# Optimization experiments

Hardware: AMD Instinct MI355X
Metric: run time of the kernel (lower is better)

Reference implementation:

```python
import jax, jax.numpy as jnp
import numpy as np

C = 256; GC = 32; G = C // GC; K = 3; S = 1; NEW = 2; PAD = (K - 1) // 2
IN1 = C * K * 2 + C * K * K // 32          # 1608
OUT1 = G * NEW * NEW * K * K // 4          # 72
OUT2 = G * NEW * NEW * K * K               # 288
B = 8; H = 56; W = 56


def setup_inputs():
    key = jax.random.key(0)
    k0, k1, k2 = jax.random.split(key, 3)
    inputs = jax.random.normal(k0, (B, C, H, W), jnp.float32)
    W1 = jax.random.normal(k1, (OUT1, IN1), jnp.float32) * np.float32(1.0 / np.sqrt(IN1))
    b1 = jnp.zeros((OUT1,), jnp.float32)
    W2 = jax.random.normal(k2, (OUT2, OUT1), jnp.float32) * np.float32(1.0 / np.sqrt(OUT1))
    b2 = jnp.zeros((OUT2,), jnp.float32)
    return {"inputs": inputs, "W1": W1, "b1": b1, "W2": W2, "b2": b2}


def _unfold(x, h, w):
    # torch.nn.Unfold(K, 1, PAD, S): patches of shape (B, C, K, K, h, w)
    xp = jnp.pad(x, ((0, 0), (0, 0), (PAD, PAD), (PAD, PAD)))
    cols = [xp[:, :, di:di + (h - 1) * S + 1:S, dj:dj + (w - 1) * S + 1:S]
            for di in range(K) for dj in range(K)]  # fixed K*K=9 slices
    return jnp.stack(cols, axis=2).reshape(x.shape[0], x.shape[1], K, K, h, w)


def reference(inputs, W1, b1, W2, b2):
    b, c, Hh, Ww = inputs.shape
    h = (Hh + 2 * PAD - K) // S + 1
    w = (Ww + 2 * PAD - K) // S + 1
    # (B, G, GC, K, K, h, w)
    x = _unfold(inputs, h, w).reshape(b, G, GC, K, K, h, w)
    # three max-pooled descriptors over different axes
    x1 = x.reshape(b, G, -1, GC // 32, K, K, h, w).max(axis=2).reshape(b, -1, h, w)  # (B, C*K*K//32, h, w)
    x2 = x.max(axis=3).reshape(b, -1, h, w)  # (B, C*K, h, w)
    x3 = x.max(axis=4).reshape(b, -1, h, w)  # (B, C*K, h, w)
    feat = jnp.concatenate([x1, x2, x3], axis=1)  # (B, IN1, h, w)
    # two biased 1x1 convs (ConvModule with no norm/act)
    y = jnp.einsum('bchw,oc->bohw', feat, W1) + b1[None, :, None, None]
    y = jnp.einsum('bchw,oc->bohw', y, W2) + b2[None, :, None, None]
    # softmax over the K*K kernel-window dim
    wgt = jax.nn.softmax(y.reshape(b, G, K * K, NEW * NEW, h, w), axis=2)
    # softmax-weighted local aggregation: sum over kernel window
    agg = jnp.einsum('bgckhw,bgknhw->bgcnhw', x.reshape(b, G, GC, K * K, h, w), wgt)
    # fold with non-overlapping (NEW, NEW) blocks == block upsampling reshape
    return agg.reshape(b, C, NEW, NEW, h, w).transpose(0, 1, 4, 2, 5, 3).reshape(b, C, h * NEW, w * NEW)
```

## Files before the change

### kernel.cpp

```cpp
#include <hip/hip_runtime.h>

#define CC   256
#define HH   56
#define WWID 56
#define KIN1 1608
#define KP1  1632
#define NO1  72
#define NO2  288
#define PPB  14
#define H2   112
#define W2D  112

typedef unsigned short u16;
typedef unsigned int   u32;
typedef __attribute__((ext_vector_type(8))) short v8s;
typedef __attribute__((ext_vector_type(4))) float v4f;

#define W1BF_ELEMS (80 * KP1)
#define W2BF_OFF_B 262144

#define LDS_TOTAL 40192
#define OFF_A 0
#define OFF_B 24832
#define OFF_C 33280
#define OFF_D 36608

__device__ __forceinline__ u16 f2b(float x) {
  u32 u = __float_as_uint(x);
  u = (u + 0x7FFFu + ((u >> 16) & 1u)) >> 16;
  return (u16)u;
}

__global__ void kConvW(const float* __restrict__ W1, const float* __restrict__ W2,
                       u16* __restrict__ w1bf, u16* __restrict__ w2bf) {
  int idx = blockIdx.x * 256 + threadIdx.x;
  if (idx < W1BF_ELEMS) {
    int m = idx / KP1, k = idx - m * KP1;
    float v = 0.f;
    if (m < NO1) {
      int orig = -1;
      if (k < 768)                 orig = 72 + (k & 255) * 3 + (k >> 8);
      else if (k < 1536)           orig = 840 + (k & 255) * 3 + ((k - 768) >> 8);
      else if ((k - 1536) < NO1)   orig = k - 1536;
      if (orig >= 0) v = W1[m * KIN1 + orig];
    }
    w1bf[idx] = f2b(v);
  } else {
    int i2 = idx - W1BF_ELEMS;
    if (i2 < NO2 * 96) {
      int m = i2 / 96, k = i2 - m * 96;
      w2bf[i2] = (k < NO1) ? f2b(W2[m * NO1 + k]) : (u16)0;
    }
  }
}

__global__ __launch_bounds__(256, 4)
void kFused(const float* __restrict__ in, const u16* __restrict__ w1bf,
            const float* __restrict__ b1, const u16* __restrict__ w2bf,
            const float* __restrict__ b2, float* __restrict__ out) {
  __shared__ __align__(16) char lds[LDS_TOTAL];
  u16*   rowmaxT = (u16*)(lds + OFF_A);
  u16*   colmaxT = (u16*)(lds + OFF_B);
  u16*   x1T     = (u16*)(lds + OFF_C);
  float* gmax_s  = (float*)(lds + OFF_D);
  float* partA   = (float*)(lds + OFF_A);
  float* y2L     = (float*)(lds + OFF_A);
  float* tile    = (float*)(lds + OFF_B);

  const int t  = threadIdx.x;
  const int jt = blockIdx.x, i = blockIdx.y, b = blockIdx.z;
  const int j0 = jt * PPB;
  const int c  = t;
  const int g  = c >> 5;
  const int gc = c & 31;
  const int w  = t >> 6, lane = t & 63;
  const int ml = lane & 15, quad = lane >> 4;

  {
    u32* xu = (u32*)x1T;
    if (t < 132) {
#pragma unroll
      for (int rp2 = 0; rp2 < 2; ++rp2) {
        int idx = 2 * t + rp2;
        if (idx < 192) { int row = idx / 12; xu[row * 52 + 36 + (idx - row * 12)] = 0u; }
        else { int e = idx - 192; xu[(14 + e / 36) * 52 + (e % 36)] = 0u; }
      }
    }
  }

  const float* rowbase0 = in + ((size_t)b * CC + c) * (HH * WWID);
  u32 win_p[3][8];
  float colmax[16];
#pragma unroll
  for (int k = 0; k < 16; ++k) colmax[k] = -3.0e38f;

#pragma unroll
  for (int r = 0; r < 3; ++r) {
    const int row = i - 1 + r;
    float sc[16];
    if (row < 0 || row >= HH) {
#pragma unroll
      for (int k = 0; k < 16; ++k) sc[k] = 0.f;
    } else {
      const float* rp = rowbase0 + row * WWID;
      float l[20];
      if (jt == 0) {
        const float4 a0 = *(const float4*)(rp), a1 = *(const float4*)(rp + 4),
                     a2 = *(const float4*)(rp + 8), a3 = *(const float4*)(rp + 12);
        l[0]=a0.x;l[1]=a0.y;l[2]=a0.z;l[3]=a0.w; l[4]=a1.x;l[5]=a1.y;l[6]=a1.z;l[7]=a1.w;
        l[8]=a2.x;l[9]=a2.y;l[10]=a2.z;l[11]=a2.w; l[12]=a3.x;l[13]=a3.y;l[14]=a3.z;l[15]=a3.w;
        sc[0] = 0.f;
#pragma unroll
        for (int k = 1; k < 16; ++k) sc[k] = l[k - 1];
      } else if (jt == 3) {
        const float* q = rp + 40;
        const float4 a0 = *(const float4*)(q), a1 = *(const float4*)(q + 4),
                     a2 = *(const float4*)(q + 8), a3 = *(const float4*)(q + 12);
        l[0]=a0.x;l[1]=a0.y;l[2]=a0.z;l[3]=a0.w; l[4]=a1.x;l[5]=a1.y;l[6]=a1.z;l[7]=a1.w;
        l[8]=a2.x;l[9]=a2.y;l[10]=a2.z;l[11]=a2.w; l[12]=a3.x;l[13]=a3.y;l[14]=a3.z;l[15]=a3.w;
#pragma unroll
        for (int k = 0; k < 15; ++k) sc[k] = l[k + 1];
        sc[15] = 0.f;
      } else {
        const float* q = rp + ((jt == 1) ? 12 : 24);
        const float4 a0 = *(const float4*)(q), a1 = *(const float4*)(q + 4),
                     a2 = *(const float4*)(q + 8), a3 = *(const float4*)(q + 12),
                     a4 = *(const float4*)(q + 16);
        l[0]=a0.x;l[1]=a0.y;l[2]=a0.z;l[3]=a0.w; l[4]=a1.x;l[5]=a1.y;l[6]=a1.z;l[7]=a1.w;
        l[8]=a2.x;l[9]=a2.y;l[10]=a2.z;l[11]=a2.w; l[12]=a3.x;l[13]=a3.y;l[14]=a3.z;l[15]=a3.w;
        l[16]=a4.x;l[17]=a4.y;l[18]=a4.z;l[19]=a4.w;
        if (jt == 1) {
#pragma unroll
          for (int k = 0; k < 16; ++k) sc[k] = l[k + 1];
        } else {
#pragma unroll
          for (int k = 0; k < 16; ++k) sc[k] = l[k + 3];
        }
      }
    }
#pragma unroll
    for (int k = 0; k < 16; ++k) colmax[k] = fmaxf(colmax[k], sc[k]);
#pragma unroll
    for (int n = 0; n < 14; ++n)
      rowmaxT[n * 776 + r * 256 + c] = f2b(fmaxf(fmaxf(sc[n], sc[n + 1]), sc[n + 2]));
#pragma unroll
    for (int col = 0; col < 16; ++col) {
      float m = sc[col];
      m = fmaxf(m, __shfl_xor(m, 1));
      m = fmaxf(m, __shfl_xor(m, 2));
      m = fmaxf(m, __shfl_xor(m, 4));
      m = fmaxf(m, __shfl_xor(m, 8));
      m = fmaxf(m, __shfl_xor(m, 16));
      if (gc == col) gmax_s[g * 48 + r * 16 + col] = m;
    }
#pragma unroll
    for (int k = 0; k < 8; ++k)
      win_p[r][k] = (u32)f2b(sc[2 * k]) | ((u32)f2b(sc[2 * k + 1]) << 16);
  }
#pragma unroll
  for (int col = 0; col < 16; ++col)
    colmaxT[col * 264 + c] = f2b(colmax[col]);
  asm volatile("s_waitcnt lgkmcnt(0)" ::: "memory");
#pragma unroll
  for (int rep = 0; rep < 4; ++rep) {
    int idx = gc + 32 * rep;
    if (idx < 126) {
      int n = idx / 9, r9 = idx - n * 9, ki = r9 / 3, kj = r9 - ki * 3;
      x1T[n * 104 + g * 9 + r9] = f2b(gmax_s[g * 48 + ki * 16 + n + kj]);
    }
  }
  __syncthreads();

  v4f acc[5];
#pragma unroll
  for (int mt = 0; mt < 5; ++mt) acc[mt] = (v4f){0.f, 0.f, 0.f, 0.f};
  const int ks0 = w * 13, ks1 = (w == 3) ? 51 : ks0 + 13;

  auto loadB = [&](int ks) -> v8s {
    if (ks < 24) {
      int kj = ks >> 3, c0 = (ks & 7) * 32;
      return *(v8s*)&colmaxT[(ml + kj) * 264 + c0 + quad * 8];
    } else if (ks < 48) {
      return *(v8s*)&rowmaxT[ml * 776 + (ks - 24) * 32 + quad * 8];
    } else {
      return *(v8s*)&x1T[ml * 104 + (ks - 48) * 32 + quad * 8];
    }
  };

  {
    v8s bf_c = loadB(ks0);
    v8s af_c[5];
    {
      const int k0 = ks0 * 32 + quad * 8;
#pragma unroll
      for (int mt = 0; mt < 5; ++mt)
        af_c[mt] = *(const v8s*)&w1bf[(mt * 16 + ml) * KP1 + k0];
    }
    for (int ks = ks0; ks < ks1; ++ks) {
      v8s bf_n, af_n[5];
      if (ks + 1 < ks1) {
        bf_n = loadB(ks + 1);
        const int k0n = (ks + 1) * 32 + quad * 8;
#pragma unroll
        for (int mt = 0; mt < 5; ++mt)
          af_n[mt] = *(const v8s*)&w1bf[(mt * 16 + ml) * KP1 + k0n];
      }
#pragma unroll
      for (int mt = 0; mt < 5; ++mt)
        acc[mt] = __builtin_amdgcn_mfma_f32_16x16x32_bf16(af_c[mt], bf_c, acc[mt], 0, 0, 0);
      if (ks + 1 < ks1) {
        bf_c = bf_n;
#pragma unroll
        for (int mt = 0; mt < 5; ++mt) af_c[mt] = af_n[mt];
      }
    }
  }
  __syncthreads();

#pragma unroll
  for (int mt = 0; mt < 5; ++mt)
    *(v4f*)&partA[((w * 5 + mt) * 16 + ml) * 16 + quad * 4] = acc[mt];
  __syncthreads();

  u16* y1b = x1T;
#pragma unroll
  for (int it = 0; it < 4; ++it) {
    int e = t + it * 256;
    if (e < NO1 * PPB) {
      int m = e / PPB, n = e - m * PPB;
      float s = b1[m];
#pragma unroll
      for (int ww = 0; ww < 4; ++ww)
        s += partA[((ww * 5 + (m >> 4)) * 16 + n) * 16 + (m & 15)];
      y1b[n * 104 + m] = f2b(s);
    }
  }
  __syncthreads();

  {
    v8s bfr[3];
#pragma unroll
    for (int ks = 0; ks < 3; ++ks)
      bfr[ks] = *(v8s*)&y1b[ml * 104 + ks * 32 + quad * 8];
    const int mt0 = (w < 2) ? 5 * w : 10 + 4 * (w - 2);
    const int mtn = (w < 2) ? 5 : 4;
    for (int mi = 0; mi < mtn; ++mi) {
      const int mt = mt0 + mi;
      v4f a2 = (v4f){0.f, 0.f, 0.f, 0.f};
#pragma unroll
      for (int ks = 0; ks < 3; ++ks) {
        v8s af = *(const v8s*)&w2bf[(mt * 16 + ml) * 96 + ks * 32 + quad * 8];
        a2 = __builtin_amdgcn_mfma_f32_16x16x32_bf16(af, bfr[ks], a2, 0, 0, 0);
      }
      const int o0 = mt * 16 + quad * 4;
      const float4 bv = *(const float4*)(b2 + o0);
      a2[0] += bv.x; a2[1] += bv.y; a2[2] += bv.z; a2[3] += bv.w;
      *(v4f*)&y2L[ml * 296 + o0] = a2;
    }
  }
  __syncthreads();

#pragma unroll
  for (int it = 0; it < 2; ++it) {
    int s2 = t + it * 256;
    if (s2 < 448) {
      int gg = s2 / 56, rem = s2 - gg * 56, nn = rem / PPB, n = rem - nn * PPB;
      float* bp = &y2L[n * 296 + gg * 36 + nn];
      float v9[9], m = -1e30f;
#pragma unroll
      for (int k = 0; k < 9; ++k) { v9[k] = bp[k * 4]; m = fmaxf(m, v9[k]); }
      float sum = 0.f;
#pragma unroll
      for (int k = 0; k < 9; ++k) { v9[k] = __expf(v9[k] - m); sum += v9[k]; }
      float inv = 1.f / sum;
#pragma unroll
      for (int k = 0; k < 9; ++k) bp[k * 4] = v9[k] * inv;
    }
  }
  __syncthreads();

  float a0s[14], a1s[14], a2s[14], a3s[14];
#pragma unroll
  for (int n = 0; n < 14; ++n) {
    const v4f* wp = (const v4f*)&y2L[n * 296 + g * 36];
    float a0 = 0.f, a1 = 0.f, a2v = 0.f, a3 = 0.f;
#pragma unroll
    for (int r = 0; r < 3; ++r) {
      float x0, x1, x2v;
      if ((n & 1) == 0) {
        u32 ua = win_p[r][n >> 1], ub = win_p[r][(n >> 1) + 1];
        x0  = __uint_as_float(ua << 16);
        x1  = __uint_as_float(ua & 0xffff0000u);
        x2v = __uint_as_float(ub << 16);
      } else {
        u32 ua = win_p[r][n >> 1], ub = win_p[r][(n >> 1) + 1];
        x0  = __uint_as_float(ua & 0xffff0000u);
        x1  = __uint_as_float(ub << 16);
        x2v = __uint_as_float(ub & 0xffff0000u);
      }
#pragma unroll
      for (int kj = 0; kj < 3; ++kj) {
        v4f wv = wp[r * 3 + kj];
        float x = (kj == 0) ? x0 : (kj == 1) ? x1 : x2v;
        a0  = fmaf(x, wv[0], a0);
        a1  = fmaf(x, wv[1], a1);
        a2v = fmaf(x, wv[2], a2v);
        a3  = fmaf(x, wv[3], a3);
      }
    }
    a0s[n] = a0; a1s[n] = a1; a2s[n] = a2v; a3s[n] = a3;
  }

  const int cl = c & 63;
  for (int ch = 0; ch < 4; ++ch) {
    if ((c >> 6) == ch) {
#pragma unroll
      for (int n = 0; n < 14; ++n) {
        float2 lo2; lo2.x = a0s[n]; lo2.y = a1s[n];
        float2 hi2; hi2.x = a2s[n]; hi2.y = a3s[n];
        *(float2*)&tile[cl * 60 + 2 * n] = lo2;
        *(float2*)&tile[cl * 60 + 28 + 2 * n] = hi2;
      }
    }
    __syncthreads();
#pragma unroll
    for (int it = 0; it < 4; ++it) {
      int f = t + it * 256;
      if (f < 896) {
        int rr = f / 7, xi = f - rr * 7;
        int cg = ch * 64 + (rr >> 1), di = rr & 1;
        v4f val = *(v4f*)&tile[(rr >> 1) * 60 + di * 28 + xi * 4];
        *(v4f*)&out[((size_t)(b * CC + cg) * H2 + (size_t)(2 * i + di)) * W2D
                    + 28 * jt + xi * 4] = val;
      }
    }
    __syncthreads();
  }
}

extern "C" void kernel_launch(void* const* d_in, const int* in_sizes, int n_in,
                              void* d_out, int out_size, void* d_ws, size_t ws_size,
                              hipStream_t stream) {
  const float* in = (const float*)d_in[0];
  const float* W1 = (const float*)d_in[1];
  const float* b1 = (const float*)d_in[2];
  const float* W2 = (const float*)d_in[3];
  const float* b2 = (const float*)d_in[4];
  float* out = (float*)d_out;

  u16* w1bf = (u16*)d_ws;
  u16* w2bf = (u16*)((char*)d_ws + W2BF_OFF_B);

  const int B = in_sizes[0] / (CC * HH * WWID);

  kConvW<<<dim3((W1BF_ELEMS + NO2 * 96 + 255) / 256), 256, 0, stream>>>(W1, W2, w1bf, w2bf);
  dim3 grid(WWID / PPB, HH, B);
  kFused<<<grid, 256, 0, stream>>>(in, w1bf, b1, w2bf, b2, out);
}
```

Before: 223.6 us.

## Widen pixel tile to 16 columns per block and restructure output transpose

Each block now covers 16 output columns instead of 14, so one MFMA N-tile of 16 is fully used instead of padded. The last column tile is partial and relies on zero padding and a bounds check on stores. The output staging is rebuilt as one full-block transpose per sub-row di, replacing four channel chunks, which cuts barriers. The cost is more registers per thread from larger window and accumulator arrays, plus wasted work in the partial tile.

```diff
diff --git a/kernel.cpp b/kernel.cpp
--- a/kernel.cpp
+++ b/kernel.cpp
@@ -7,7 +7,7 @@
 #define KP1  1632
 #define NO1  72
 #define NO2  288
-#define PPB  14
+#define PPB  16
 #define H2   112
 #define W2D  112
 
@@ -19,11 +19,11 @@
 #define W1BF_ELEMS (80 * KP1)
 #define W2BF_OFF_B 262144
 
-#define LDS_TOTAL 40192
-#define OFF_A 0
-#define OFF_B 24832
-#define OFF_C 33280
-#define OFF_D 36608
+#define LDS_TOTAL 39392
+#define OFF_ROW 0
+#define OFF_COL 24832
+#define OFF_X1  34336
+#define OFF_GMX 37664
 
 __device__ __forceinline__ u16 f2b(float x) {
   u32 u = __float_as_uint(x);
@@ -54,119 +54,108 @@
   }
 }
 
-__global__ __launch_bounds__(256, 4)
+__global__ __launch_bounds__(256) __attribute__((amdgpu_waves_per_eu(4, 4)))
 void kFused(const float* __restrict__ in, const u16* __restrict__ w1bf,
             const float* __restrict__ b1, const u16* __restrict__ w2bf,
             const float* __restrict__ b2, float* __restrict__ out) {
   __shared__ __align__(16) char lds[LDS_TOTAL];
-  u16*   rowmaxT = (u16*)(lds + OFF_A);
-  u16*   colmaxT = (u16*)(lds + OFF_B);
-  u16*   x1T     = (u16*)(lds + OFF_C);
-  float* gmax_s  = (float*)(lds + OFF_D);
-  float* partA   = (float*)(lds + OFF_A);
-  float* y2L     = (float*)(lds + OFF_A);
-  float* tile    = (float*)(lds + OFF_B);
+  u16*   rowmaxT = (u16*)(lds + OFF_ROW);
+  u16*   colmaxT = (u16*)(lds + OFF_COL);
+  u16*   x1T     = (u16*)(lds + OFF_X1);
+  float* gmax_s  = (float*)(lds + OFF_GMX);
+  float* partA   = (float*)lds;
+  float* y2L     = (float*)lds;
+  float* tile    = (float*)lds;
 
   const int t  = threadIdx.x;
   const int jt = blockIdx.x, i = blockIdx.y, b = blockIdx.z;
-  const int j0 = jt * PPB;
-  const int c  = t;
-  const int g  = c >> 5;
-  const int gc = c & 31;
+  const int g  = t >> 5;
   const int w  = t >> 6, lane = t & 63;
   const int ml = lane & 15, quad = lane >> 4;
 
-  {
+  if (t < 192) {
     u32* xu = (u32*)x1T;
-    if (t < 132) {
-#pragma unroll
-      for (int rp2 = 0; rp2 < 2; ++rp2) {
-        int idx = 2 * t + rp2;
-        if (idx < 192) { int row = idx / 12; xu[row * 52 + 36 + (idx - row * 12)] = 0u; }
-        else { int e = idx - 192; xu[(14 + e / 36) * 52 + (e % 36)] = 0u; }
-      }
-    }
-  }
-
-  const float* rowbase0 = in + ((size_t)b * CC + c) * (HH * WWID);
-  u32 win_p[3][8];
-  float colmax[16];
-#pragma unroll
-  for (int k = 0; k < 16; ++k) colmax[k] = -3.0e38f;
+    xu[(t / 12) * 52 + 36 + (t % 12)] = 0u;
+  }
+
+  const float* rowbase0 = in + ((size_t)b * CC + t) * (HH * WWID);
+  u32 win_p[3][9];
+  float colmax[18];
+#pragma unroll
+  for (int k = 0; k < 18; ++k) colmax[k] = -3.0e38f;
 
 #pragma unroll
   for (int r = 0; r < 3; ++r) {
     const int row = i - 1 + r;
-    float sc[16];
+    float sc[18];
     if (row < 0 || row >= HH) {
 #pragma unroll
-      for (int k = 0; k < 16; ++k) sc[k] = 0.f;
+      for (int k = 0; k < 18; ++k) sc[k] = 0.f;
     } else {
       const float* rp = rowbase0 + row * WWID;
-      float l[20];
       if (jt == 0) {
-        const float4 a0 = *(const float4*)(rp), a1 = *(const float4*)(rp + 4),
-                     a2 = *(const float4*)(rp + 8), a3 = *(const float4*)(rp + 12);
-        l[0]=a0.x;l[1]=a0.y;l[2]=a0.z;l[3]=a0.w; l[4]=a1.x;l[5]=a1.y;l[6]=a1.z;l[7]=a1.w;
-        l[8]=a2.x;l[9]=a2.y;l[10]=a2.z;l[11]=a2.w; l[12]=a3.x;l[13]=a3.y;l[14]=a3.z;l[15]=a3.w;
-        sc[0] = 0.f;
-#pragma unroll
-        for (int k = 1; k < 16; ++k) sc[k] = l[k - 1];
-      } else if (jt == 3) {
-        const float* q = rp + 40;
-        const float4 a0 = *(const float4*)(q), a1 = *(const float4*)(q + 4),
-                     a2 = *(const float4*)(q + 8), a3 = *(const float4*)(q + 12);
-        l[0]=a0.x;l[1]=a0.y;l[2]=a0.z;l[3]=a0.w; l[4]=a1.x;l[5]=a1.y;l[6]=a1.z;l[7]=a1.w;
-        l[8]=a2.x;l[9]=a2.y;l[10]=a2.z;l[11]=a2.w; l[12]=a3.x;l[13]=a3.y;l[14]=a3.z;l[15]=a3.w;
-#pragma unroll
-        for (int k = 0; k < 15; ++k) sc[k] = l[k + 1];
-        sc[15] = 0.f;
-      } else {
-        const float* q = rp + ((jt == 1) ? 12 : 24);
-        const float4 a0 = *(const float4*)(q), a1 = *(const float4*)(q + 4),
-                     a2 = *(const float4*)(q + 8), a3 = *(const float4*)(q + 12),
-                     a4 = *(const float4*)(q + 16);
+        float l[20];
+        const float4 a0 = *(const float4*)(rp),      a1 = *(const float4*)(rp + 4),
+                     a2 = *(const float4*)(rp + 8),  a3 = *(const float4*)(rp + 12),
+                     a4 = *(const float4*)(rp + 16);
         l[0]=a0.x;l[1]=a0.y;l[2]=a0.z;l[3]=a0.w; l[4]=a1.x;l[5]=a1.y;l[6]=a1.z;l[7]=a1.w;
         l[8]=a2.x;l[9]=a2.y;l[10]=a2.z;l[11]=a2.w; l[12]=a3.x;l[13]=a3.y;l[14]=a3.z;l[15]=a3.w;
         l[16]=a4.x;l[17]=a4.y;l[18]=a4.z;l[19]=a4.w;
-        if (jt == 1) {
-#pragma unroll
-          for (int k = 0; k < 16; ++k) sc[k] = l[k + 1];
-        } else {
-#pragma unroll
-          for (int k = 0; k < 16; ++k) sc[k] = l[k + 3];
-        }
-      }
-    }
-#pragma unroll
-    for (int k = 0; k < 16; ++k) colmax[k] = fmaxf(colmax[k], sc[k]);
-#pragma unroll
-    for (int n = 0; n < 14; ++n)
-      rowmaxT[n * 776 + r * 256 + c] = f2b(fmaxf(fmaxf(sc[n], sc[n + 1]), sc[n + 2]));
-#pragma unroll
-    for (int col = 0; col < 16; ++col) {
+        sc[0] = 0.f;
+#pragma unroll
+        for (int k = 1; k < 18; ++k) sc[k] = l[k - 1];
+      } else if (jt == 3) {
+        float l[12];
+        const float4 a0 = *(const float4*)(rp + 44), a1 = *(const float4*)(rp + 48),
+                     a2 = *(const float4*)(rp + 52);
+        l[0]=a0.x;l[1]=a0.y;l[2]=a0.z;l[3]=a0.w; l[4]=a1.x;l[5]=a1.y;l[6]=a1.z;l[7]=a1.w;
+        l[8]=a2.x;l[9]=a2.y;l[10]=a2.z;l[11]=a2.w;
+#pragma unroll
+        for (int k = 0; k < 18; ++k) sc[k] = (k <= 8) ? l[k + 3] : 0.f;
+      } else {
+        float l[24];
+        const float* q = rp + ((jt == 1) ? 12 : 28);
+        const float4 a0 = *(const float4*)(q),      a1 = *(const float4*)(q + 4),
+                     a2 = *(const float4*)(q + 8),  a3 = *(const float4*)(q + 12),
+                     a4 = *(const float4*)(q + 16), a5 = *(const float4*)(q + 20);
+        l[0]=a0.x;l[1]=a0.y;l[2]=a0.z;l[3]=a0.w; l[4]=a1.x;l[5]=a1.y;l[6]=a1.z;l[7]=a1.w;
+        l[8]=a2.x;l[9]=a2.y;l[10]=a2.z;l[11]=a2.w; l[12]=a3.x;l[13]=a3.y;l[14]=a3.z;l[15]=a3.w;
+        l[16]=a4.x;l[17]=a4.y;l[18]=a4.z;l[19]=a4.w; l[20]=a5.x;l[21]=a5.y;l[22]=a5.z;l[23]=a5.w;
+#pragma unroll
+        for (int k = 0; k < 18; ++k) sc[k] = l[k + 3];
+      }
+    }
+#pragma unroll
+    for (int k = 0; k < 18; ++k) colmax[k] = fmaxf(colmax[k], sc[k]);
+#pragma unroll
+    for (int n = 0; n < 16; ++n)
+      rowmaxT[n * 776 + r * 256 + t] = f2b(fmaxf(fmaxf(sc[n], sc[n + 1]), sc[n + 2]));
+#pragma unroll
+    for (int col = 0; col < 18; ++col) {
       float m = sc[col];
       m = fmaxf(m, __shfl_xor(m, 1));
       m = fmaxf(m, __shfl_xor(m, 2));
       m = fmaxf(m, __shfl_xor(m, 4));
       m = fmaxf(m, __shfl_xor(m, 8));
       m = fmaxf(m, __shfl_xor(m, 16));
-      if (gc == col) gmax_s[g * 48 + r * 16 + col] = m;
-    }
-#pragma unroll
-    for (int k = 0; k < 8; ++k)
+      if ((t & 31) == col) gmax_s[g * 54 + r * 18 + col] = m;
+    }
+#pragma unroll
+    for (int k = 0; k < 9; ++k)
       win_p[r][k] = (u32)f2b(sc[2 * k]) | ((u32)f2b(sc[2 * k + 1]) << 16);
   }
 #pragma unroll
-  for (int col = 0; col < 16; ++col)
-    colmaxT[col * 264 + c] = f2b(colmax[col]);
+  for (int col = 0; col < 18; ++col)
+    colmaxT[col * 264 + t] = f2b(colmax[col]);
   asm volatile("s_waitcnt lgkmcnt(0)" ::: "memory");
 #pragma unroll
-  for (int rep = 0; rep < 4; ++rep) {
-    int idx = gc + 32 * rep;
-    if (idx < 126) {
-      int n = idx / 9, r9 = idx - n * 9, ki = r9 / 3, kj = r9 - ki * 3;
-      x1T[n * 104 + g * 9 + r9] = f2b(gmax_s[g * 48 + ki * 16 + n + kj]);
+  for (int rep = 0; rep < 5; ++rep) {
+    int idx = lane + 64 * rep;
+    if (idx < 288) {
+      int gl = idx / 144, rem = idx - gl * 144;
+      int n = rem / 9, r9 = rem - n * 9, ki = r9 / 3, kj = r9 - ki * 3;
+      int gg = 2 * w + gl;
+      x1T[n * 104 + gg * 9 + r9] = f2b(gmax_s[gg * 54 + ki * 18 + n + kj]);
     }
   }
   __syncthreads();
@@ -224,10 +213,10 @@
 
   u16* y1b = x1T;
 #pragma unroll
-  for (int it = 0; it < 4; ++it) {
+  for (int it = 0; it < 5; ++it) {
     int e = t + it * 256;
-    if (e < NO1 * PPB) {
-      int m = e / PPB, n = e - m * PPB;
+    if (e < NO1 * 16) {
+      int m = e >> 4, n = e & 15;
       float s = b1[m];
 #pragma unroll
       for (int ww = 0; ww < 4; ++ww)
@@ -263,37 +252,34 @@
 #pragma unroll
   for (int it = 0; it < 2; ++it) {
     int s2 = t + it * 256;
-    if (s2 < 448) {
-      int gg = s2 / 56, rem = s2 - gg * 56, nn = rem / PPB, n = rem - nn * PPB;
-      float* bp = &y2L[n * 296 + gg * 36 + nn];
-      float v9[9], m = -1e30f;
-#pragma unroll
-      for (int k = 0; k < 9; ++k) { v9[k] = bp[k * 4]; m = fmaxf(m, v9[k]); }
-      float sum = 0.f;
-#pragma unroll
-      for (int k = 0; k < 9; ++k) { v9[k] = __expf(v9[k] - m); sum += v9[k]; }
-      float inv = 1.f / sum;
-#pragma unroll
-      for (int k = 0; k < 9; ++k) bp[k * 4] = v9[k] * inv;
-    }
-  }
-  __syncthreads();
-
-  float a0s[14], a1s[14], a2s[14], a3s[14];
-#pragma unroll
-  for (int n = 0; n < 14; ++n) {
+    int gg = s2 >> 6, rem = s2 & 63, nn = rem >> 4, n = rem & 15;
+    float* bp = &y2L[n * 296 + gg * 36 + nn];
+    float v9[9], m = -1e30f;
+#pragma unroll
+    for (int k = 0; k < 9; ++k) { v9[k] = bp[k * 4]; m = fmaxf(m, v9[k]); }
+    float sum = 0.f;
+#pragma unroll
+    for (int k = 0; k < 9; ++k) { v9[k] = __expf(v9[k] - m); sum += v9[k]; }
+    float inv = 1.f / sum;
+#pragma unroll
+    for (int k = 0; k < 9; ++k) bp[k * 4] = v9[k] * inv;
+  }
+  __syncthreads();
+
+  float a0s[16], a1s[16], a2s[16], a3s[16];
+#pragma unroll
+  for (int n = 0; n < 16; ++n) {
     const v4f* wp = (const v4f*)&y2L[n * 296 + g * 36];
     float a0 = 0.f, a1 = 0.f, a2v = 0.f, a3 = 0.f;
 #pragma unroll
     for (int r = 0; r < 3; ++r) {
       float x0, x1, x2v;
+      u32 ua = win_p[r][n >> 1], ub = win_p[r][(n >> 1) + 1];
       if ((n & 1) == 0) {
-        u32 ua = win_p[r][n >> 1], ub = win_p[r][(n >> 1) + 1];
         x0  = __uint_as_float(ua << 16);
         x1  = __uint_as_float(ua & 0xffff0000u);
         x2v = __uint_as_float(ub << 16);
       } else {
-        u32 ua = win_p[r][n >> 1], ub = win_p[r][(n >> 1) + 1];
         x0  = __uint_as_float(ua & 0xffff0000u);
         x1  = __uint_as_float(ub << 16);
         x2v = __uint_as_float(ub & 0xffff0000u);
@@ -310,31 +296,28 @@
     }
     a0s[n] = a0; a1s[n] = a1; a2s[n] = a2v; a3s[n] = a3;
   }
-
-  const int cl = c & 63;
-  for (int ch = 0; ch < 4; ++ch) {
-    if ((c >> 6) == ch) {
-#pragma unroll
-      for (int n = 0; n < 14; ++n) {
-        float2 lo2; lo2.x = a0s[n]; lo2.y = a1s[n];
-        float2 hi2; hi2.x = a2s[n]; hi2.y = a3s[n];
-        *(float2*)&tile[cl * 60 + 2 * n] = lo2;
-        *(float2*)&tile[cl * 60 + 28 + 2 * n] = hi2;
-      }
+  __syncthreads();
+
+  for (int di = 0; di < 2; ++di) {
+#pragma unroll
+    for (int n = 0; n < 16; ++n) {
+      tile[(2 * n) * 258 + t]     = di ? a2s[n] : a0s[n];
+      tile[(2 * n + 1) * 258 + t] = di ? a3s[n] : a1s[n];
     }
     __syncthreads();
 #pragma unroll
-    for (int it = 0; it < 4; ++it) {
+    for (int it = 0; it < 8; ++it) {
       int f = t + it * 256;
-      if (f < 896) {
-        int rr = f / 7, xi = f - rr * 7;
-        int cg = ch * 64 + (rr >> 1), di = rr & 1;
-        v4f val = *(v4f*)&tile[(rr >> 1) * 60 + di * 28 + xi * 4];
-        *(v4f*)&out[((size_t)(b * CC + cg) * H2 + (size_t)(2 * i + di)) * W2D
-                    + 28 * jt + xi * 4] = val;
-      }
-    }
-    __syncthreads();
+      int c = f >> 3, fx = f & 7;
+      int xcol = 32 * jt + fx * 4;
+      if (xcol < W2D) {
+        v4f v;
+#pragma unroll
+        for (int s = 0; s < 4; ++s) v[s] = tile[(fx * 4 + s) * 258 + c];
+        *(v4f*)&out[((size_t)(b * CC + c) * H2 + (size_t)(2 * i + di)) * W2D + xcol] = v;
+      }
+    }
+    if (di == 0) __syncthreads();
   }
 }
 
@@ -354,6 +337,6 @@
   const int B = in_sizes[0] / (CC * HH * WWID);
 
   kConvW<<<dim3((W1BF_ELEMS + NO2 * 96 + 255) / 256), 256, 0, stream>>>(W1, W2, w1bf, w2bf);
-  dim3 grid(WWID / PPB, HH, B);
+  dim3 grid(4, HH, B);
   kFused<<<grid, 256, 0, stream>>>(in, w1bf, b1, w2bf, b2, out);
 }
```

Result: slower. 603.7 us (+170.0%).
